# Kernel optimization log

Hardware: AMD Instinct MI355X
Metric: run time of the kernel (lower is better)

The kernel has to match this reference:

```python
import jax, jax.numpy as jnp
import numpy as np

B, S, D, H = 64, 512, 1024, 1024


def setup_inputs() -> dict:
    key = jax.random.key(0)
    k1, k2, k3 = jax.random.split(key, 3)
    x = jax.random.normal(k1, (B, S, D), dtype=jnp.float32)
    # torch nn.Linear weight: [4H, D+H], bias: [4H]; scale ~ U-like small init
    W = jax.random.normal(k2, (4 * H, D + H), dtype=jnp.float32) * (1.0 / np.sqrt(D + H))
    b = jax.random.normal(k3, (4 * H,), dtype=jnp.float32) * 0.01
    return {"x": x, "W": W, "b": b}


def reference(x, W, b):
    """BaselineLSTM forward (use_ln=False, dropout=Identity).

    Returns (outputs [B,S,H], (h [B,H], c [B,H])).
    """
    Bv, Sv, Dv = x.shape
    Hv = W.shape[0] // 4
    h0 = jnp.zeros((Bv, Hv), dtype=x.dtype)
    c0 = jnp.zeros((Bv, Hv), dtype=x.dtype)

    def step(carry, x_t):
        h, c = carry
        # gates = Linear(cat([x_t, h])) -> [B, 4H], chunk order i,f,o,g
        gates = jnp.concatenate([x_t, h], axis=1) @ W.T + b
        i, f, o, g = jnp.split(gates, 4, axis=1)
        c_new = jax.nn.sigmoid(f) * c + jax.nn.sigmoid(i) * jnp.tanh(g)
        h_new = jax.nn.sigmoid(o) * jnp.tanh(c_new)
        return (h_new, c_new), h_new

    (h, c), outs = jax.lax.scan(step, (h0, c0), jnp.swapaxes(x, 0, 1))
    outputs = jnp.swapaxes(outs, 0, 1)  # [B, S, H]
    return outputs, (h, c)
```

## Files before the change

kernel.cpp:

```cpp
#include <hip/hip_runtime.h>

typedef unsigned short ushort_t;
typedef unsigned long long u64_t;
typedef float  f32x4  __attribute__((ext_vector_type(4)));
typedef __bf16 bf16x8 __attribute__((ext_vector_type(8)));

#define NB   64
#define NS   512
#define ND   1024
#define NH   1024
#define NG   4096

__device__ __forceinline__ ushort_t f2bf(float f) {
  unsigned u = __float_as_uint(f);
  u += 0x7FFFu + ((u >> 16) & 1u);
  return (ushort_t)(u >> 16);
}
__device__ __forceinline__ float bf2f(ushort_t u) {
  return __uint_as_float(((unsigned)u) << 16);
}
__device__ __forceinline__ float sigmoid_f(float x) {
  return 1.0f / (1.0f + __expf(-x));
}
__device__ __forceinline__ float tanh_f(float x) {
  return 1.0f - 2.0f / (__expf(2.0f * x) + 1.0f);
}

__global__ __launch_bounds__(256) void cvt_x_kernel(const float4* __restrict__ x,
                                                    ushort_t* __restrict__ xb) {
  int i = blockIdx.x * 256 + threadIdx.x;
  float4 v = x[i];
  ushort4 o;
  o.x = f2bf(v.x); o.y = f2bf(v.y); o.z = f2bf(v.z); o.w = f2bf(v.w);
  *(ushort4*)(xb + (size_t)i * 4) = o;
}

__global__ __launch_bounds__(256) void cvt_w_kernel(const float4* __restrict__ W,
                                                    ushort_t* __restrict__ Wx,
                                                    ushort_t* __restrict__ Wh) {
  int i = blockIdx.x * 256 + threadIdx.x;
  float4 v = W[i];
  int e = i * 4;
  int n = e >> 11;
  int c = e & 2047;
  ushort4 o;
  o.x = f2bf(v.x); o.y = f2bf(v.y); o.z = f2bf(v.z); o.w = f2bf(v.w);
  ushort_t* dst = (c < ND) ? (Wx + (size_t)n * ND + c)
                           : (Wh + (size_t)n * NH + (c - ND));
  *(ushort4*)dst = o;
}

__global__ __launch_bounds__(256) void pregemm_kernel(
    const ushort_t* __restrict__ xb, const ushort_t* __restrict__ Wx,
    const float* __restrict__ bias, ushort_t* __restrict__ PG) {
  int bid  = blockIdx.x;
  int mblk = bid >> 5;
  int nblk = bid & 31;
  int tid  = threadIdx.x;
  int lane = tid & 63, w = tid >> 6;
  int l15  = lane & 15, q = lane >> 4;
  int row0 = mblk * 128 + (w >> 1) * 64;
  int col0 = nblk * 128 + (w & 1) * 64;
  const ushort_t* aBase = xb + (size_t)(row0 + l15) * ND + q * 8;
  const ushort_t* bBase = Wx + (size_t)(col0 + l15) * ND + q * 8;

  f32x4 acc[4][4] = {};
#pragma unroll 2
  for (int k0 = 0; k0 < ND; k0 += 32) {
    bf16x8 a[4], b[4];
#pragma unroll
    for (int mi = 0; mi < 4; ++mi)
      a[mi] = *reinterpret_cast<const bf16x8*>(aBase + (size_t)mi * 16 * ND + k0);
#pragma unroll
    for (int ni = 0; ni < 4; ++ni)
      b[ni] = *reinterpret_cast<const bf16x8*>(bBase + (size_t)ni * 16 * ND + k0);
#pragma unroll
    for (int mi = 0; mi < 4; ++mi)
#pragma unroll
      for (int ni = 0; ni < 4; ++ni)
        acc[mi][ni] = __builtin_amdgcn_mfma_f32_16x16x32_bf16(a[mi], b[ni], acc[mi][ni], 0, 0, 0);
  }
#pragma unroll
  for (int ni = 0; ni < 4; ++ni) {
    int n = col0 + ni * 16 + l15;
    float bv = bias[n];
#pragma unroll
    for (int mi = 0; mi < 4; ++mi) {
#pragma unroll
      for (int r = 0; r < 4; ++r) {
        int m  = row0 + mi * 16 + q * 4 + r;
        int bb = m >> 9;
        int t  = m & 511;
        PG[((size_t)t * NB + bb) * NG + n] = f2bf(acc[mi][ni][r] + bv);
      }
    }
  }
}

__global__ __launch_bounds__(1024) void lstm_rec_kernel(
    const ushort_t* __restrict__ PG, const ushort_t* __restrict__ Wh,
    ushort_t* hbuf, unsigned* flags, float* __restrict__ out) {
  __shared__ ushort_t lds_h[16 * 1024];
  __shared__ float lds_g[4][16][66];

  int bid  = blockIdx.x;
  int mach = bid >> 4;
  int slot = bid & 15;
  int tid  = threadIdx.x;
  int lane = tid & 63, w = tid >> 6;
  int g = w & 3, jb = w >> 2;
  int l15 = lane & 15, q = lane >> 4;
  int mb = tid >> 6, jc = tid & 63;

  ushort_t* hm0 = hbuf + (size_t)(mach * 2) * (16 * NH);
  ushort_t* hm1 = hm0 + 16 * NH;

  const ushort_t* bB =
      Wh + (size_t)(g * NH + slot * 64 + jb * 16 + l15) * NH + q * 8;

  int swA = (l15 & 7) << 4;
  const char* aRow = (const char*)lds_h + l15 * 2048;

  unsigned* myflag = flags + (size_t)(mach * 16 + slot) * 32;
  float c_reg = 0.f;

  int bglob = mach * 16 + mb;
  int jglob = slot * 64 + jc;

  ushort_t pg0, pg1, pg2, pg3;
  {
    const ushort_t* pp = PG + (size_t)bglob * NG + jglob;
    pg0 = __builtin_nontemporal_load(pp);
    pg1 = __builtin_nontemporal_load(pp + NH);
    pg2 = __builtin_nontemporal_load(pp + 2 * NH);
    pg3 = __builtin_nontemporal_load(pp + 3 * NH);
  }

  for (int t = 0; t < NS; ++t) {
    if (t > 0) {
      if (w == 0) {
        unsigned tgt = (unsigned)t;
        const unsigned* fp = flags + (size_t)(mach * 16 + (lane & 15)) * 32;
        int guard = 0;
        for (;;) {
          unsigned v = __hip_atomic_load(fp, __ATOMIC_RELAXED,
                                         __HIP_MEMORY_SCOPE_AGENT);
          if (__all(v >= tgt)) break;
          if (++guard > (1 << 14)) break;
        }
      }
      __builtin_amdgcn_sched_barrier(0);
      __syncthreads();
    }

    {
      const u64_t* hb64 =
          (const u64_t*)((t & 1) ? hm1 : hm0);
      u64_t hv8[4];
#pragma unroll
      for (int it = 0; it < 4; ++it)
        hv8[it] = __hip_atomic_load(hb64 + it * 1024 + tid,
                                    __ATOMIC_RELAXED, __HIP_MEMORY_SCOPE_AGENT);
#pragma unroll
      for (int it = 0; it < 4; ++it) {
        int idx  = it * 1024 + tid;
        int row  = idx >> 8;
        int colB = (idx & 255) * 8;
        *(u64_t*)((char*)lds_h + row * 2048 + (colB ^ ((row & 7) << 4))) = hv8[it];
      }
    }
    __syncthreads();

    f32x4 acc = {};
#pragma unroll 8
    for (int k0 = 0; k0 < NH; k0 += 32) {
      bf16x8 av = *(const bf16x8*)(aRow + ((16 * q + 2 * k0) ^ swA));
      bf16x8 bv = *reinterpret_cast<const bf16x8*>(bB + k0);
      acc = __builtin_amdgcn_mfma_f32_16x16x32_bf16(av, bv, acc, 0, 0, 0);
    }
#pragma unroll
    for (int r = 0; r < 4; ++r)
      lds_g[g][q * 4 + r][jb * 16 + l15] = acc[r];
    __syncthreads();

    float gi = lds_g[0][mb][jc] + bf2f(pg0);
    float gf = lds_g[1][mb][jc] + bf2f(pg1);
    float go = lds_g[2][mb][jc] + bf2f(pg2);
    float gg = lds_g[3][mb][jc] + bf2f(pg3);
    float cn = sigmoid_f(gf) * c_reg + sigmoid_f(gi) * tanh_f(gg);
    float hv = sigmoid_f(go) * tanh_f(cn);
    c_reg = cn;

    unsigned my16 = (unsigned)f2bf(hv);
    unsigned nb16 = (unsigned)__shfl_down((int)my16, 1);
    if (t == NS - 1) {
      out[((size_t)bglob * NS + t) * NH + jglob] = hv;
      out[(size_t)NB * NS * NH + (size_t)bglob * NH + jglob] = hv;
      out[(size_t)NB * NS * NH + (size_t)NB * NH + (size_t)bglob * NH + jglob] = cn;
    } else {
      if ((tid & 1) == 0) {
        unsigned* hn32 = (unsigned*)((t & 1) ? hm0 : hm1);
        __hip_atomic_store(hn32 + mb * 512 + slot * 32 + (jc >> 1),
                           my16 | (nb16 << 16),
                           __ATOMIC_RELAXED, __HIP_MEMORY_SCOPE_AGENT);
      }
      __syncthreads();
      if (tid == 0)
        __hip_atomic_store(myflag, (unsigned)(t + 1),
                           __ATOMIC_RELAXED, __HIP_MEMORY_SCOPE_AGENT);
      __builtin_nontemporal_store(hv, &out[((size_t)bglob * NS + t) * NH + jglob]);
      const ushort_t* pn = PG + ((size_t)(t + 1) * NB + bglob) * NG + jglob;
      pg0 = __builtin_nontemporal_load(pn);
      pg1 = __builtin_nontemporal_load(pn + NH);
      pg2 = __builtin_nontemporal_load(pn + 2 * NH);
      pg3 = __builtin_nontemporal_load(pn + 3 * NH);
    }
  }
}

extern "C" void kernel_launch(void* const* d_in, const int* in_sizes, int n_in,
                              void* d_out, int out_size, void* d_ws, size_t ws_size,
                              hipStream_t stream) {
  const float* x    = (const float*)d_in[0];
  const float* W    = (const float*)d_in[1];
  const float* bias = (const float*)d_in[2];
  float* out = (float*)d_out;

  const size_t off_hbuf  = 0;
  const size_t off_flags = 262144;
  const size_t off_Wx    = 270336;
  const size_t off_Wh    = off_Wx + 8388608;
  const size_t off_xb    = off_Wh + 8388608;
  const size_t off_PG    = off_xb + 67108864;
  const size_t need      = off_PG + 268435456;
  if (ws_size < need) return;

  char* ws = (char*)d_ws;
  ushort_t* hbuf  = (ushort_t*)(ws + off_hbuf);
  unsigned* flags = (unsigned*)(ws + off_flags);
  ushort_t* Wx    = (ushort_t*)(ws + off_Wx);
  ushort_t* Wh    = (ushort_t*)(ws + off_Wh);
  ushort_t* xb    = (ushort_t*)(ws + off_xb);
  ushort_t* PG    = (ushort_t*)(ws + off_PG);

  hipMemsetAsync(ws, 0, 270336, stream);

  cvt_x_kernel<<<32768, 256, 0, stream>>>((const float4*)x, xb);
  cvt_w_kernel<<<8192, 256, 0, stream>>>((const float4*)W, Wx, Wh);
  pregemm_kernel<<<8192, 256, 0, stream>>>(xb, Wx, bias, PG);

  void* args[] = { (void*)&PG, (void*)&Wh, (void*)&hbuf, (void*)&flags, (void*)&out };
  hipLaunchCooperativeKernel((void*)lstm_rec_kernel, dim3(64), dim3(1024),
                             args, 0, stream);
}
```

Measured before the change: 9.533 ms.

## Replace per-block flags with step-tagged hidden-state words for inter-block sync

Each hidden value is now published as a 32-bit word holding the bf16 value and a step tag, so consumers poll the hidden buffer itself until every word carries the expected tag. This removes the separate flag store, the barrier before it and the flag-polling round trip, taking the release/acquire chain off the per-step critical path. In exchange each block reads twice as many bytes per step and spins on the full buffer, and correctness relies on relaxed atomic 32-bit stores being observed whole without explicit fences.

```diff
diff --git a/kernel.cpp b/kernel.cpp
--- a/kernel.cpp
+++ b/kernel.cpp
@@ -99,7 +99,7 @@
 
 __global__ __launch_bounds__(1024) void lstm_rec_kernel(
     const ushort_t* __restrict__ PG, const ushort_t* __restrict__ Wh,
-    ushort_t* hbuf, unsigned* flags, float* __restrict__ out) {
+    unsigned* hbuf, float* __restrict__ out) {
   __shared__ ushort_t lds_h[16 * 1024];
   __shared__ float lds_g[4][16][66];
 
@@ -112,8 +112,7 @@
   int l15 = lane & 15, q = lane >> 4;
   int mb = tid >> 6, jc = tid & 63;
 
-  ushort_t* hm0 = hbuf + (size_t)(mach * 2) * (16 * NH);
-  ushort_t* hm1 = hm0 + 16 * NH;
+  unsigned* hm = hbuf + (size_t)mach * 2 * 16384;
 
   const ushort_t* bB =
       Wh + (size_t)(g * NH + slot * 64 + jb * 16 + l15) * NH + q * 8;
@@ -121,7 +120,6 @@
   int swA = (l15 & 7) << 4;
   const char* aRow = (const char*)lds_h + l15 * 2048;
 
-  unsigned* myflag = flags + (size_t)(mach * 16 + slot) * 32;
   float c_reg = 0.f;
 
   int bglob = mach * 16 + mb;
@@ -137,36 +135,34 @@
   }
 
   for (int t = 0; t < NS; ++t) {
-    if (t > 0) {
-      if (w == 0) {
-        unsigned tgt = (unsigned)t;
-        const unsigned* fp = flags + (size_t)(mach * 16 + (lane & 15)) * 32;
-        int guard = 0;
-        for (;;) {
-          unsigned v = __hip_atomic_load(fp, __ATOMIC_RELAXED,
-                                         __HIP_MEMORY_SCOPE_AGENT);
-          if (__all(v >= tgt)) break;
-          if (++guard > (1 << 14)) break;
+    {
+      const u64_t* hb64 = (const u64_t*)(hm + (t & 1) * 16384);
+      u64_t v[8];
+      unsigned tg = (unsigned)t;
+      int guard = 0;
+      bool ok = false;
+      while (!ok) {
+#pragma unroll
+        for (int it = 0; it < 8; ++it)
+          v[it] = __hip_atomic_load(hb64 + it * 1024 + tid,
+                                    __ATOMIC_RELAXED, __HIP_MEMORY_SCOPE_AGENT);
+        ok = true;
+#pragma unroll
+        for (int it = 0; it < 8; ++it) {
+          unsigned t0 = ((unsigned)(v[it] >> 16)) & 0xffffu;
+          unsigned t1 = (unsigned)(v[it] >> 48);
+          ok = ok && (t0 == tg) && (t1 == tg);
         }
+        if (++guard > (1 << 12)) break;
       }
-      __builtin_amdgcn_sched_barrier(0);
-      __syncthreads();
-    }
-
-    {
-      const u64_t* hb64 =
-          (const u64_t*)((t & 1) ? hm1 : hm0);
-      u64_t hv8[4];
-#pragma unroll
-      for (int it = 0; it < 4; ++it)
-        hv8[it] = __hip_atomic_load(hb64 + it * 1024 + tid,
-                                    __ATOMIC_RELAXED, __HIP_MEMORY_SCOPE_AGENT);
-#pragma unroll
-      for (int it = 0; it < 4; ++it) {
-        int idx  = it * 1024 + tid;
-        int row  = idx >> 8;
-        int colB = (idx & 255) * 8;
-        *(u64_t*)((char*)lds_h + row * 2048 + (colB ^ ((row & 7) << 4))) = hv8[it];
+#pragma unroll
+      for (int it = 0; it < 8; ++it) {
+        int idx = 2 * (it * 1024 + tid);
+        int row = idx >> 10;
+        int j0  = idx & 1023;
+        unsigned val = ((unsigned)v[it] & 0xffffu) |
+                       ((((unsigned)(v[it] >> 32)) & 0xffffu) << 16);
+        *(unsigned*)((char*)lds_h + row * 2048 + ((j0 * 2) ^ ((row & 7) << 4))) = val;
       }
     }
     __syncthreads();
@@ -191,23 +187,15 @@
     float hv = sigmoid_f(go) * tanh_f(cn);
     c_reg = cn;
 
-    unsigned my16 = (unsigned)f2bf(hv);
-    unsigned nb16 = (unsigned)__shfl_down((int)my16, 1);
     if (t == NS - 1) {
       out[((size_t)bglob * NS + t) * NH + jglob] = hv;
       out[(size_t)NB * NS * NH + (size_t)bglob * NH + jglob] = hv;
       out[(size_t)NB * NS * NH + (size_t)NB * NH + (size_t)bglob * NH + jglob] = cn;
     } else {
-      if ((tid & 1) == 0) {
-        unsigned* hn32 = (unsigned*)((t & 1) ? hm0 : hm1);
-        __hip_atomic_store(hn32 + mb * 512 + slot * 32 + (jc >> 1),
-                           my16 | (nb16 << 16),
-                           __ATOMIC_RELAXED, __HIP_MEMORY_SCOPE_AGENT);
-      }
-      __syncthreads();
-      if (tid == 0)
-        __hip_atomic_store(myflag, (unsigned)(t + 1),
-                           __ATOMIC_RELAXED, __HIP_MEMORY_SCOPE_AGENT);
+      unsigned pub = (unsigned)f2bf(hv) | (((unsigned)(t + 1)) << 16);
+      unsigned* hn = hm + ((t + 1) & 1) * 16384;
+      __hip_atomic_store(hn + mb * 1024 + jglob, pub,
+                         __ATOMIC_RELAXED, __HIP_MEMORY_SCOPE_AGENT);
       __builtin_nontemporal_store(hv, &out[((size_t)bglob * NS + t) * NH + jglob]);
       const ushort_t* pn = PG + ((size_t)(t + 1) * NB + bglob) * NG + jglob;
       pg0 = __builtin_nontemporal_load(pn);
@@ -226,30 +214,28 @@
   const float* bias = (const float*)d_in[2];
   float* out = (float*)d_out;
 
-  const size_t off_hbuf  = 0;
-  const size_t off_flags = 262144;
-  const size_t off_Wx    = 270336;
-  const size_t off_Wh    = off_Wx + 8388608;
-  const size_t off_xb    = off_Wh + 8388608;
-  const size_t off_PG    = off_xb + 67108864;
-  const size_t need      = off_PG + 268435456;
+  const size_t off_hbuf = 0;
+  const size_t off_Wx   = 524288;
+  const size_t off_Wh   = off_Wx + 8388608;
+  const size_t off_xb   = off_Wh + 8388608;
+  const size_t off_PG   = off_xb + 67108864;
+  const size_t need     = off_PG + 268435456;
   if (ws_size < need) return;
 
   char* ws = (char*)d_ws;
-  ushort_t* hbuf  = (ushort_t*)(ws + off_hbuf);
-  unsigned* flags = (unsigned*)(ws + off_flags);
-  ushort_t* Wx    = (ushort_t*)(ws + off_Wx);
-  ushort_t* Wh    = (ushort_t*)(ws + off_Wh);
-  ushort_t* xb    = (ushort_t*)(ws + off_xb);
-  ushort_t* PG    = (ushort_t*)(ws + off_PG);
-
-  hipMemsetAsync(ws, 0, 270336, stream);
+  unsigned* hbuf = (unsigned*)(ws + off_hbuf);
+  ushort_t* Wx   = (ushort_t*)(ws + off_Wx);
+  ushort_t* Wh   = (ushort_t*)(ws + off_Wh);
+  ushort_t* xb   = (ushort_t*)(ws + off_xb);
+  ushort_t* PG   = (ushort_t*)(ws + off_PG);
+
+  hipMemsetAsync(ws, 0, 524288, stream);
 
   cvt_x_kernel<<<32768, 256, 0, stream>>>((const float4*)x, xb);
   cvt_w_kernel<<<8192, 256, 0, stream>>>((const float4*)W, Wx, Wh);
   pregemm_kernel<<<8192, 256, 0, stream>>>(xb, Wx, bias, PG);
 
-  void* args[] = { (void*)&PG, (void*)&Wh, (void*)&hbuf, (void*)&flags, (void*)&out };
+  void* args[] = { (void*)&PG, (void*)&Wh, (void*)&hbuf, (void*)&out };
   hipLaunchCooperativeKernel((void*)lstm_rec_kernel, dim3(64), dim3(1024),
                              args, 0, stream);
 }
```

Result: slower. 9.885 ms (+3.7%).
